# Kernel optimization log

Measured on AMD Instinct MI355X. Metric: run time of the kernel, lower is better.

## Reference

```python
import jax, jax.numpy as jnp
import numpy as np

N = 16384   # nodes
E = 131072  # edges (avg degree 8)
F = 64      # channels (hidden_irreps scalar multiplicity)
K = 16      # spherical harmonic components, l=0..3
Z = 10      # num_elements
G = 64      # graphs in batch
NB = 8      # num_bessel
RMAX = 5.0
P = 5       # num_polynomial_cutoff
AVG = 8.0   # avg_num_neighbors


def _sph(u):
    # real spherical harmonics l=0..3, 'component' normalization, unit input u [E,3]
    x, y, z = u[..., 0], u[..., 1], u[..., 2]
    s3, s5, s7 = 3.0 ** 0.5, 5.0 ** 0.5, 7.0 ** 0.5
    s15, s21, s35, s105 = 15.0 ** 0.5, 21.0 ** 0.5, 35.0 ** 0.5, 105.0 ** 0.5
    Y = [jnp.ones_like(x),
         s3 * x, s3 * y, s3 * z,
         s15 * x * y, s15 * y * z, 0.5 * s5 * (3.0 * z * z - 1.0), s15 * x * z,
         0.5 * s15 * (x * x - y * y),
         0.25 * s35 * y * (3.0 * x * x - y * y), 0.5 * s105 * x * y * z,
         0.25 * s21 * y * (5.0 * z * z - 1.0), 0.5 * s7 * z * (5.0 * z * z - 3.0),
         0.25 * s21 * x * (5.0 * z * z - 1.0), 0.25 * s105 * z * (x * x - y * y),
         0.25 * s35 * x * (x * x - 3.0 * y * y)]
    return jnp.stack(Y, axis=-1)  # [E,16]


def _radial(lengths):
    # Bessel basis * polynomial cutoff envelope (p=5)
    u = lengths / RMAX
    n = jnp.arange(1, NB + 1, dtype=lengths.dtype)
    safe = jnp.maximum(lengths, 1e-6)
    bess = (2.0 / RMAX) ** 0.5 * jnp.sin(n * jnp.pi * u[:, None]) / safe[:, None]
    env = (1.0 - 0.5 * (P + 1) * (P + 2) * u ** P + P * (P + 2) * u ** (P + 1)
           - 0.5 * P * (P + 1) * u ** (P + 2))
    env = env * (u < 1.0).astype(lengths.dtype)
    return bess * env[:, None]  # [E,NB]


def setup_inputs() -> dict:
    key = jax.random.key(0)
    ks = jax.random.split(key, 16)
    d = {}
    d['positions'] = jax.random.normal(ks[0], (N, 3), jnp.float32) * 1.5
    d['atomic_energies'] = jax.random.normal(ks[1], (Z,), jnp.float32)
    d['W_embed'] = jax.random.normal(ks[2], (Z, F), jnp.float32)
    d['rW1'] = jax.random.normal(ks[3], (2, NB, 64), jnp.float32) / NB ** 0.5
    d['rW2'] = jax.random.normal(ks[4], (2, 64, 64), jnp.float32) / 8.0
    d['rW3'] = jax.random.normal(ks[5], (2, 64, 64), jnp.float32) / 8.0
    d['rWout'] = jax.random.normal(ks[6], (2, 64, K * F), jnp.float32) / 8.0
    d['Wsc'] = jax.random.normal(ks[7], (2, Z, F, F), jnp.float32) / F ** 0.5
    d['pw'] = jax.random.normal(ks[8], (2, 3, F), jnp.float32) * 0.1
    d['read1_w'] = jax.random.normal(ks[9], (F,), jnp.float32) / F ** 0.5
    d['read2_Wa'] = jax.random.normal(ks[10], (F, 16), jnp.float32) / F ** 0.5
    d['read2_wb'] = jax.random.normal(ks[11], (16,), jnp.float32) / 4.0
    d['species'] = jax.random.randint(ks[12], (N,), 0, Z, jnp.int32)
    d['edge_index'] = jax.random.randint(ks[13], (2, E), 0, N, jnp.int32)
    d['batch'] = jnp.sort(jax.random.randint(ks[14], (N,), 0, G, jnp.int32))
    return d


def reference(positions, atomic_energies, W_embed, rW1, rW2, rW3, rWout, Wsc, pw,
              read1_w, read2_Wa, read2_wb, species, edge_index, batch):
    silu = jax.nn.silu
    src, dst = edge_index[0], edge_index[1]
    vec = positions[dst] - positions[src]                       # [E,3]
    lengths = jnp.sqrt(jnp.sum(vec * vec, axis=-1) + 1e-12)
    unit = vec / lengths[:, None]
    Y = _sph(unit)                                              # [E,K]
    edge_feats = _radial(lengths)                               # [E,NB]

    onehot = jax.nn.one_hot(species, Z, dtype=positions.dtype)  # node_attrs
    node_e0 = atomic_energies[species]                          # AtomicEnergiesBlock
    h = jnp.zeros((N, K, F), positions.dtype).at[:, 0, :].set(onehot @ W_embed)

    node_es = node_e0
    for l in range(2):  # num_interactions (structurally fixed small loop)
        # radial MLP [NB]->64->64->64->K*F, per-edge tensor-product weights
        R = silu(silu(silu(edge_feats @ rW1[l]) @ rW2[l]) @ rW3[l]) @ rWout[l]
        R = R.reshape(E, K, F)
        # gather -> channelwise tensor product with spherical harmonics -> scatter
        m = R * Y[:, :, None] * h[src, 0, :][:, None, :]        # [E,K,F]
        A = jax.ops.segment_sum(m, dst, num_segments=N) / AVG   # [N,K,F]
        # element-dependent skip connection (residual sc)
        sc = jnp.einsum('nkc,ncd->nkd', h, Wsc[l][species])
        # symmetric product basis (correlation up to 3) -> invariant contractions
        inv2 = jnp.sum(A * A, axis=1)                           # [N,F]
        inv3 = inv2 * A[:, 0, :]
        h_new = A * pw[l, 0][None, None, :]
        h_new = h_new.at[:, 0, :].add(inv2 * pw[l, 1] + inv3 * pw[l, 2])
        h = h_new + sc
        if l == 0:
            node_es = node_es + h[:, 0, :] @ read1_w            # LinearReadoutBlock
        else:
            node_es = node_es + silu(h[:, 0, :] @ read2_Wa) @ read2_wb  # NonLinearReadout
    total_energy = jax.ops.segment_sum(node_es, batch, num_segments=G)  # [G]
    return total_energy
```

## Files before the change

kernel.cpp:

```cpp
#include <hip/hip_runtime.h>
#include <math.h>


#define NN 16384
#define NE 131072
#define NZ 10
#define NG 64

typedef __attribute__((ext_vector_type(8))) short bf16x8;
typedef __attribute__((ext_vector_type(4))) float f32x4;

__device__ __forceinline__ float silu_f(float x) {
    return x / (1.0f + __expf(-x));
}

__device__ __forceinline__ unsigned short f2bf_rne(float x) {
    unsigned int u = __float_as_uint(x);
    unsigned int r = (u + 0x7FFFu + ((u >> 16) & 1u)) >> 16;
    return (unsigned short)r;
}
__device__ __forceinline__ float bf2f(unsigned short b) {
    return __uint_as_float(((unsigned int)b) << 16);
}

__global__ __launch_bounds__(256) void k_count(
    const int* __restrict__ ei, int* __restrict__ deg)
{
    int e = blockIdx.x * 256 + threadIdx.x;
    if (e < NE) atomicAdd(&deg[ei[NE + e]], 1);
}

__global__ __launch_bounds__(256) void k_scan(
    const int* __restrict__ deg, int* __restrict__ cursor)
{
    __shared__ int part[256];
    int t = threadIdx.x;
    int base = t * 64;
    int s = 0;
    for (int i = 0; i < 64; i++) s += deg[base + i];
    part[t] = s;
    __syncthreads();
    for (int off = 1; off < 256; off <<= 1) {
        int v = (t >= off) ? part[t - off] : 0;
        __syncthreads();
        part[t] += v;
        __syncthreads();
    }
    int run = (t > 0) ? part[t - 1] : 0;
    for (int i = 0; i < 64; i++) { cursor[base + i] = run; run += deg[base + i]; }
}

__global__ __launch_bounds__(256) void k_fill(
    const int* __restrict__ ei, int* __restrict__ cursor,
    int* __restrict__ sSrc, int* __restrict__ sDst)
{
    int e = blockIdx.x * 256 + threadIdx.x;
    if (e >= NE) return;
    int d = ei[NE + e];
    int p = atomicAdd(&cursor[d], 1);
    sSrc[p] = ei[e];
    sDst[p] = d;
}

__global__ __launch_bounds__(256) void k_wprep(
    const float* __restrict__ Wout, unsigned short* __restrict__ Bh,
    unsigned short* __restrict__ Bl)
{
    int idx = blockIdx.x * 256 + threadIdx.x;
    int lane = idx & 63;
    int nb = (idx >> 6) & 63;
    int ks = (idx >> 12) & 1;
    int layer = idx >> 13;
    int col = nb * 16 + (lane & 15);
    int tbase = ks * 32 + ((lane >> 4) << 3);
    #pragma unroll
    for (int j = 0; j < 8; j++) {
        float v = Wout[(size_t)layer * 65536 + (size_t)(tbase + j) * 1024 + col];
        unsigned short hi = f2bf_rne(v);
        unsigned short lo = f2bf_rne(v - bf2f(hi));
        Bh[(size_t)idx * 8 + j] = hi;
        Bl[(size_t)idx * 8 + j] = lo;
    }
}

__global__ __launch_bounds__(256) void k_edge_geom(
    const float* __restrict__ pos, const int* __restrict__ sSrc,
    const int* __restrict__ sDst, float* __restrict__ Y, float* __restrict__ feats)
{
    int e = blockIdx.x * 256 + threadIdx.x;
    if (e >= NE) return;
    int s = sSrc[e];
    int d = sDst[e];
    float vx = pos[d*3+0] - pos[s*3+0];
    float vy = pos[d*3+1] - pos[s*3+1];
    float vz = pos[d*3+2] - pos[s*3+2];
    float len = sqrtf(vx*vx + vy*vy + vz*vz + 1e-12f);
    float inv = 1.0f / len;
    float x = vx*inv, y = vy*inv, z = vz*inv;

    const float s3 = 1.7320508075688772f, s5 = 2.2360679774997896f;
    const float s7 = 2.6457513110645907f, s15 = 3.872983346207417f;
    const float s21 = 4.58257569495584f, s35 = 5.916079783099616f;
    const float s105 = 10.246950765959598f;
    float xx = x*x, yy = y*y, zz = z*z;
    float* Ye = Y + (size_t)e*16;
    Ye[0] = 1.0f;
    Ye[1] = s3*x; Ye[2] = s3*y; Ye[3] = s3*z;
    Ye[4] = s15*x*y; Ye[5] = s15*y*z; Ye[6] = 0.5f*s5*(3.0f*zz - 1.0f);
    Ye[7] = s15*x*z; Ye[8] = 0.5f*s15*(xx - yy);
    Ye[9]  = 0.25f*s35*y*(3.0f*xx - yy);
    Ye[10] = 0.5f*s105*x*y*z;
    Ye[11] = 0.25f*s21*y*(5.0f*zz - 1.0f);
    Ye[12] = 0.5f*s7*z*(5.0f*zz - 3.0f);
    Ye[13] = 0.25f*s21*x*(5.0f*zz - 1.0f);
    Ye[14] = 0.25f*s105*z*(xx - yy);
    Ye[15] = 0.25f*s35*x*(xx - 3.0f*yy);

    float u = len * 0.2f;
    float safe = fmaxf(len, 1e-6f);
    float u5 = u*u; u5 = u5*u5*u;
    float env = 1.0f - 21.0f*u5 + 35.0f*u5*u - 15.0f*u5*u*u;
    env = (u < 1.0f) ? env : 0.0f;
    float c = 0.6324555320336759f * env / safe;
    float* fe = feats + (size_t)e*8;
    const float PI = 3.14159265358979323846f;
    #pragma unroll
    for (int n = 1; n <= 8; n++)
        fe[n-1] = c * __sinf((float)n * PI * u);
}

__global__ __launch_bounds__(256) void k_h_init(
    const float* __restrict__ W_embed, const float* __restrict__ ae,
    const int* __restrict__ species, float* __restrict__ h0,
    float* __restrict__ node_es)
{
    int i = blockIdx.x * 256 + threadIdx.x;
    int n = i >> 6, r = i & 63;
    int sp = species[n];
    h0[i] = W_embed[sp*64 + r];
    if (r == 0) node_es[n] = ae[sp];
}

__global__ __launch_bounds__(256) void k_radial(
    const float* __restrict__ feats, const float* __restrict__ rW1,
    const float* __restrict__ rW2, const float* __restrict__ rW3,
    float* __restrict__ T3)
{
    __shared__ float w1[8*64];
    __shared__ float w2[64*64];
    __shared__ float w3[64*64];
    __shared__ float act[4][64];
    for (int i = threadIdx.x; i < 8*64; i += 256) w1[i] = rW1[i];
    for (int i = threadIdx.x; i < 64*64; i += 256) { w2[i] = rW2[i]; w3[i] = rW3[i]; }
    __syncthreads();
    int wave = threadIdx.x >> 6, lane = threadIdx.x & 63;
    for (int e0 = blockIdx.x * 4; e0 < NE; e0 += gridDim.x * 4) {
        int e = e0 + wave;
        const float* fe = feats + (size_t)e*8;
        float a = 0.f;
        #pragma unroll
        for (int i = 0; i < 8; i++) a = fmaf(fe[i], w1[i*64+lane], a);
        a = silu_f(a);
        act[wave][lane] = a;
        float b = 0.f;
        #pragma unroll
        for (int i = 0; i < 64; i++) b = fmaf(act[wave][i], w2[i*64+lane], b);
        b = silu_f(b);
        act[wave][lane] = b;
        float cc = 0.f;
        #pragma unroll
        for (int i = 0; i < 64; i++) cc = fmaf(act[wave][i], w3[i*64+lane], cc);
        T3[(size_t)e*64 + lane] = silu_f(cc);
    }
}

__global__ __launch_bounds__(256) void k_message(
    const float* __restrict__ T3, const unsigned short* __restrict__ Bh,
    const unsigned short* __restrict__ Bl, const float* __restrict__ Y,
    const float* __restrict__ h, const int* __restrict__ sSrc,
    const int* __restrict__ sDst, float* __restrict__ A)
{
    __shared__ float mbuf[16][518];
    __shared__ float hs[16][64];
    __shared__ float ys[16][16];
    __shared__ int srcs[16];
    __shared__ int dsts[16];

    int tid = threadIdx.x;
    int lane = tid & 63;
    int w = tid >> 6;
    int tile0 = blockIdx.x * 64;
    const bf16x8* Bhf = (const bf16x8*)Bh;
    const bf16x8* Blf = (const bf16x8*)Bl;

    int prev_d = -1, run_start = 0;
    float r00 = 0.f, r01 = 0.f, r10 = 0.f, r11 = 0.f;

    for (int sb = 0; sb < 4; sb++) {
        int g0 = tile0 + sb * 16;
        __syncthreads();
        if (tid < 16) { srcs[tid] = sSrc[g0 + tid]; dsts[tid] = sDst[g0 + tid]; }

        const float* trow = T3 + (size_t)(g0 + (lane & 15)) * 64 + ((lane >> 4) << 3);
        float4 p0 = *(const float4*)(trow);
        float4 p1 = *(const float4*)(trow + 4);
        float4 p2 = *(const float4*)(trow + 32);
        float4 p3 = *(const float4*)(trow + 36);
        bf16x8 ah0, al0, ah1, al1;
        {
            float v[16] = {p0.x,p0.y,p0.z,p0.w, p1.x,p1.y,p1.z,p1.w,
                           p2.x,p2.y,p2.z,p2.w, p3.x,p3.y,p3.z,p3.w};
            #pragma unroll
            for (int j = 0; j < 8; j++) {
                unsigned short hi = f2bf_rne(v[j]);
                ah0[j] = (short)hi;
                al0[j] = (short)f2bf_rne(v[j] - bf2f(hi));
            }
            #pragma unroll
            for (int j = 0; j < 8; j++) {
                unsigned short hi = f2bf_rne(v[8+j]);
                ah1[j] = (short)hi;
                al1[j] = (short)f2bf_rne(v[8+j] - bf2f(hi));
            }
        }
        __syncthreads();
        {
            int row = tid >> 4, q = tid & 15;
            ((float4*)hs[row])[q] = ((const float4*)(h + (size_t)srcs[row] * 64))[q];
            ys[row][q] = Y[(size_t)(g0 + row) * 16 + q];
        }
        __syncthreads();

        float hv[4][4];
        #pragma unroll
        for (int r = 0; r < 4; r++)
            #pragma unroll
            for (int m4 = 0; m4 < 4; m4++)
                hv[r][m4] = hs[(lane >> 4) * 4 + r][m4 * 16 + (lane & 15)];

        auto merge = [&](int p, float& r0, float& r1, int& pd_io, int& rs_io) {
            int pd = pd_io, rs = rs_io;
            #pragma unroll 1
            for (int e = 0; e < 16; e++) {
                int g = sb * 16 + e;
                int d = dsts[e];
                if (g == 0) {
                    pd = d;
                } else if (d != pd) {
                    float* Ap = A + (size_t)pd * 1024 + p * 512 + 2 * tid;
                    if (rs == 0) { atomicAdd(Ap, r0); atomicAdd(Ap + 1, r1); }
                    else         { *(float2*)Ap = make_float2(r0, r1); }
                    r0 = 0.f; r1 = 0.f; rs = g; pd = d;
                }
                float2 v = *(const float2*)&mbuf[e][2 * tid];
                r0 += v.x; r1 += v.y;
            }
            pd_io = pd; rs_io = rs;
        };

        for (int p = 0; p < 2; p++) {
            float yv[4][2];
            #pragma unroll
            for (int r = 0; r < 4; r++)
                #pragma unroll
                for (int kk = 0; kk < 2; kk++)
                    yv[r][kk] = ys[(lane >> 4) * 4 + r][p * 8 + w * 2 + kk] * 0.125f;

            #pragma unroll
            for (int nbl = 0; nbl < 8; nbl++) {
                int nb = p * 32 + w * 8 + nbl;
                bf16x8 bh0 = Bhf[(0 * 64 + nb) * 64 + lane];
                bf16x8 bl0 = Blf[(0 * 64 + nb) * 64 + lane];
                bf16x8 bh1 = Bhf[(1 * 64 + nb) * 64 + lane];
                bf16x8 bl1 = Blf[(1 * 64 + nb) * 64 + lane];
                f32x4 acc = {0.f, 0.f, 0.f, 0.f};
                acc = __builtin_amdgcn_mfma_f32_16x16x32_bf16(ah0, bh0, acc, 0, 0, 0);
                acc = __builtin_amdgcn_mfma_f32_16x16x32_bf16(al0, bh0, acc, 0, 0, 0);
                acc = __builtin_amdgcn_mfma_f32_16x16x32_bf16(ah0, bl0, acc, 0, 0, 0);
                acc = __builtin_amdgcn_mfma_f32_16x16x32_bf16(ah1, bh1, acc, 0, 0, 0);
                acc = __builtin_amdgcn_mfma_f32_16x16x32_bf16(al1, bh1, acc, 0, 0, 0);
                acc = __builtin_amdgcn_mfma_f32_16x16x32_bf16(ah1, bl1, acc, 0, 0, 0);
                #pragma unroll
                for (int r = 0; r < 4; r++) {
                    float m = acc[r] * yv[r][nbl >> 2] * hv[r][nbl & 3];
                    mbuf[(lane >> 4) * 4 + r][(w * 8 + nbl) * 16 + (lane & 15)] = m;
                }
            }
            __syncthreads();
            if (p == 0) {
                int pd0 = prev_d, rs0 = run_start;
                merge(0, r00, r01, pd0, rs0);
            } else {
                merge(1, r10, r11, prev_d, run_start);
            }
            __syncthreads();
        }
    }
    {
        float* Ap = A + (size_t)prev_d * 1024 + 2 * tid;
        atomicAdd(Ap, r00); atomicAdd(Ap + 1, r01);
        float* Ap1 = A + (size_t)prev_d * 1024 + 512 + 2 * tid;
        atomicAdd(Ap1, r10); atomicAdd(Ap1 + 1, r11);
    }
}

__global__ __launch_bounds__(256) void k_update0(
    const float* __restrict__ A, const float* __restrict__ h0,
    const float* __restrict__ Wsc, const float* __restrict__ pw,
    const float* __restrict__ read1_w, const int* __restrict__ species,
    float* __restrict__ h2, float* __restrict__ node_es)
{
    __shared__ float h0s[4][64];
    int wave = threadIdx.x >> 6, lane = threadIdx.x & 63;
    int n = blockIdx.x * 4 + wave;
    h0s[wave][lane] = h0[(size_t)n*64 + lane];
    __syncthreads();
    int sp = species[n];
    const float* W = Wsc + (size_t)sp*4096;
    float sc0 = 0.f;
    #pragma unroll
    for (int c = 0; c < 64; c++) sc0 = fmaf(h0s[wave][c], W[c*64+lane], sc0);
    float a[16], inv2 = 0.f;
    #pragma unroll
    for (int kk = 0; kk < 16; kk++) {
        a[kk] = A[(size_t)n*1024 + kk*64 + lane];
        inv2 = fmaf(a[kk], a[kk], inv2);
    }
    float inv3 = inv2 * a[0];
    float hn0 = a[0]*pw[lane] + inv2*pw[64+lane] + inv3*pw[128+lane] + sc0;
    h2[(size_t)n*64 + lane] = hn0;
    float r = hn0 * read1_w[lane];
    #pragma unroll
    for (int off = 32; off; off >>= 1) r += __shfl_down(r, off, 64);
    if (lane == 0) node_es[n] += r;
}

__global__ __launch_bounds__(256) void k_update1(
    const float* __restrict__ A, const float* __restrict__ h2,
    const float* __restrict__ Wsc, const float* __restrict__ pw,
    const float* __restrict__ Wa, const float* __restrict__ wb,
    const int* __restrict__ species, float* __restrict__ node_es)
{
    __shared__ float h0s[4][64];
    __shared__ float hns[4][64];
    int wave = threadIdx.x >> 6, lane = threadIdx.x & 63;
    int n = blockIdx.x * 4 + wave;
    h0s[wave][lane] = h2[(size_t)n*64 + lane];
    __syncthreads();
    int sp = species[n];
    const float* W = Wsc + (size_t)sp*4096;
    float sc0 = 0.f;
    #pragma unroll
    for (int c = 0; c < 64; c++) sc0 = fmaf(h0s[wave][c], W[c*64+lane], sc0);
    float a[16], inv2 = 0.f;
    #pragma unroll
    for (int kk = 0; kk < 16; kk++) {
        a[kk] = A[(size_t)n*1024 + kk*64 + lane];
        inv2 = fmaf(a[kk], a[kk], inv2);
    }
    float inv3 = inv2 * a[0];
    float hn0 = a[0]*pw[lane] + inv2*pw[64+lane] + inv3*pw[128+lane] + sc0;
    hns[wave][lane] = hn0;
    __syncthreads();
    float contrib = 0.f;
    if (lane < 16) {
        float aj = 0.f;
        #pragma unroll
        for (int f = 0; f < 64; f++) aj = fmaf(hns[wave][f], Wa[f*16+lane], aj);
        contrib = silu_f(aj) * wb[lane];
    }
    #pragma unroll
    for (int off = 8; off; off >>= 1) contrib += __shfl_down(contrib, off, 64);
    if (lane == 0) node_es[n] += contrib;
}

__global__ __launch_bounds__(256) void k_reduce(
    const float* __restrict__ node_es, const int* __restrict__ batch,
    float* __restrict__ out)
{
    __shared__ float bins[NG];
    if (threadIdx.x < NG) bins[threadIdx.x] = 0.f;
    __syncthreads();
    for (int n = blockIdx.x*256 + threadIdx.x; n < NN; n += gridDim.x*256)
        atomicAdd(&bins[batch[n]], node_es[n]);
    __syncthreads();
    if (threadIdx.x < NG) atomicAdd(&out[threadIdx.x], bins[threadIdx.x]);
}

extern "C" void kernel_launch(void* const* d_in, const int* in_sizes, int n_in,
                              void* d_out, int out_size, void* d_ws, size_t ws_size,
                              hipStream_t stream)
{
    const float* positions = (const float*)d_in[0];
    const float* atomic_energies = (const float*)d_in[1];
    const float* W_embed  = (const float*)d_in[2];
    const float* rW1      = (const float*)d_in[3];
    const float* rW2      = (const float*)d_in[4];
    const float* rW3      = (const float*)d_in[5];
    const float* rWout    = (const float*)d_in[6];
    const float* Wsc      = (const float*)d_in[7];
    const float* pw       = (const float*)d_in[8];
    const float* read1_w  = (const float*)d_in[9];
    const float* read2_Wa = (const float*)d_in[10];
    const float* read2_wb = (const float*)d_in[11];
    const int* species    = (const int*)d_in[12];
    const int* edge_index = (const int*)d_in[13];
    const int* batch      = (const int*)d_in[14];
    float* out = (float*)d_out;

    char* w = (char*)d_ws;
    float* Y     = (float*)w;  w += (size_t)NE*16*4;
    float* feats = (float*)w;  w += (size_t)NE*8*4;
    float* T3    = (float*)w;  w += (size_t)NE*64*4;
    float* h0    = (float*)w;  w += (size_t)NN*64*4;
    float* h2    = (float*)w;  w += (size_t)NN*64*4;
    float* A     = (float*)w;  w += (size_t)NN*1024*4;
    float* node_es = (float*)w; w += (size_t)NN*4;
    int* deg     = (int*)w;    w += (size_t)NN*4;
    int* cursor  = (int*)w;    w += (size_t)NN*4;
    int* sSrc    = (int*)w;    w += (size_t)NE*4;
    int* sDst    = (int*)w;    w += (size_t)NE*4;
    unsigned short* Bh = (unsigned short*)w; w += (size_t)2*8192*8*2;
    unsigned short* Bl = (unsigned short*)w; w += (size_t)2*8192*8*2;

    hipMemsetAsync(deg, 0, (size_t)NN*4, stream);
    k_count<<<NE/256, 256, 0, stream>>>(edge_index, deg);
    k_scan<<<1, 256, 0, stream>>>(deg, cursor);
    k_fill<<<NE/256, 256, 0, stream>>>(edge_index, cursor, sSrc, sDst);

    k_wprep<<<64, 256, 0, stream>>>(rWout, Bh, Bl);
    k_edge_geom<<<NE/256, 256, 0, stream>>>(positions, sSrc, sDst, Y, feats);
    k_h_init<<<NN*64/256, 256, 0, stream>>>(W_embed, atomic_energies, species, h0, node_es);

    hipMemsetAsync(A, 0, (size_t)NN*1024*4, stream);
    k_radial<<<2048, 256, 0, stream>>>(feats, rW1, rW2, rW3, T3);
    k_message<<<NE/64, 256, 0, stream>>>(T3, Bh, Bl, Y, h0, sSrc, sDst, A);
    k_update0<<<NN/4, 256, 0, stream>>>(A, h0, Wsc, pw, read1_w, species, h2, node_es);

    hipMemsetAsync(A, 0, (size_t)NN*1024*4, stream);
    k_radial<<<2048, 256, 0, stream>>>(feats, rW1 + 8*64, rW2 + 64*64, rW3 + 64*64, T3);
    k_message<<<NE/64, 256, 0, stream>>>(T3, Bh + (size_t)8192*8, Bl + (size_t)8192*8,
                                         Y, h2, sSrc, sDst, A);
    k_update1<<<NN/4, 256, 0, stream>>>(A, h2, Wsc + 10*4096, pw + 192,
                                        read2_Wa, read2_wb, species, node_es);

    hipMemsetAsync(d_out, 0, NG*sizeof(float), stream);
    k_reduce<<<64, 256, 0, stream>>>(node_es, batch, out);
}
```

Before: 726.6 us.

## Reduce message runs in registers via shuffles instead of LDS staging buffer

The 33KB LDS message buffer and its two-phase merge loop are removed. Destination runs over the 64-edge tile are now precomputed once, and each MFMA output is reduced into per-run register carries using cross-lane shuffles, then written or atomically added to A directly. Dropping the large LDS buffer allows a higher occupancy hint (launch_bounds 256,4) and removes several barriers per sub-block. In exchange it adds a serial run-scan loop with branching per MFMA tile, extra shuffles, and more narrow 16-lane global stores.

```diff
diff --git a/kernel.cpp b/kernel.cpp
--- a/kernel.cpp
+++ b/kernel.cpp
@@ -174,34 +174,55 @@
     }
 }
 
-__global__ __launch_bounds__(256) void k_message(
+__global__ __launch_bounds__(256, 4) void k_message(
     const float* __restrict__ T3, const unsigned short* __restrict__ Bh,
     const unsigned short* __restrict__ Bl, const float* __restrict__ Y,
     const float* __restrict__ h, const int* __restrict__ sSrc,
     const int* __restrict__ sDst, float* __restrict__ A)
 {
-    __shared__ float mbuf[16][518];
     __shared__ float hs[16][64];
     __shared__ float ys[16][16];
     __shared__ int srcs[16];
-    __shared__ int dsts[16];
+    __shared__ int dall[64];
+    __shared__ int runs_s[65];
+    __shared__ int runs_d[64];
+    __shared__ int nruns_sh;
 
     int tid = threadIdx.x;
     int lane = tid & 63;
     int w = tid >> 6;
+    int gq = lane >> 4;
+    int cl = lane & 15;
     int tile0 = blockIdx.x * 64;
     const bf16x8* Bhf = (const bf16x8*)Bh;
     const bf16x8* Blf = (const bf16x8*)Bl;
 
-    int prev_d = -1, run_start = 0;
-    float r00 = 0.f, r01 = 0.f, r10 = 0.f, r11 = 0.f;
+    if (tid < 64) dall[tid] = sDst[tile0 + tid];
+    __syncthreads();
+    if (tid == 0) {
+        int nr = 0, prev = -1;
+        for (int e = 0; e < 64; e++) {
+            int d = dall[e];
+            if (d != prev) { runs_s[nr] = e; runs_d[nr] = d; prev = d; nr++; }
+        }
+        runs_s[nr] = 64;
+        nruns_sh = nr;
+    }
+    __syncthreads();
+
+    float carry[2][8];
+    #pragma unroll
+    for (int p = 0; p < 2; p++)
+        #pragma unroll
+        for (int q = 0; q < 8; q++) carry[p][q] = 0.f;
+
+    int run_lo = 0;
 
     for (int sb = 0; sb < 4; sb++) {
-        int g0 = tile0 + sb * 16;
-        __syncthreads();
-        if (tid < 16) { srcs[tid] = sSrc[g0 + tid]; dsts[tid] = sDst[g0 + tid]; }
-
-        const float* trow = T3 + (size_t)(g0 + (lane & 15)) * 64 + ((lane >> 4) << 3);
+        int S = sb * 16;
+        int g0 = tile0 + S;
+
+        const float* trow = T3 + (size_t)(g0 + cl) * 64 + (gq << 3);
         float4 p0 = *(const float4*)(trow);
         float4 p1 = *(const float4*)(trow + 4);
         float4 p2 = *(const float4*)(trow + 32);
@@ -223,6 +244,9 @@
                 al1[j] = (short)f2bf_rne(v[8+j] - bf2f(hi));
             }
         }
+
+        __syncthreads();
+        if (tid < 16) srcs[tid] = sSrc[g0 + tid];
         __syncthreads();
         {
             int row = tid >> 4, q = tid & 15;
@@ -236,43 +260,26 @@
         for (int r = 0; r < 4; r++)
             #pragma unroll
             for (int m4 = 0; m4 < 4; m4++)
-                hv[r][m4] = hs[(lane >> 4) * 4 + r][m4 * 16 + (lane & 15)];
-
-        auto merge = [&](int p, float& r0, float& r1, int& pd_io, int& rs_io) {
-            int pd = pd_io, rs = rs_io;
-            #pragma unroll 1
-            for (int e = 0; e < 16; e++) {
-                int g = sb * 16 + e;
-                int d = dsts[e];
-                if (g == 0) {
-                    pd = d;
-                } else if (d != pd) {
-                    float* Ap = A + (size_t)pd * 1024 + p * 512 + 2 * tid;
-                    if (rs == 0) { atomicAdd(Ap, r0); atomicAdd(Ap + 1, r1); }
-                    else         { *(float2*)Ap = make_float2(r0, r1); }
-                    r0 = 0.f; r1 = 0.f; rs = g; pd = d;
-                }
-                float2 v = *(const float2*)&mbuf[e][2 * tid];
-                r0 += v.x; r1 += v.y;
-            }
-            pd_io = pd; rs_io = rs;
-        };
-
+                hv[r][m4] = hs[gq*4 + r][m4*16 + cl];
+
+        while (runs_s[run_lo + 1] <= S) run_lo++;
+
+        #pragma unroll
         for (int p = 0; p < 2; p++) {
             float yv[4][2];
             #pragma unroll
             for (int r = 0; r < 4; r++)
                 #pragma unroll
                 for (int kk = 0; kk < 2; kk++)
-                    yv[r][kk] = ys[(lane >> 4) * 4 + r][p * 8 + w * 2 + kk] * 0.125f;
+                    yv[r][kk] = ys[gq*4 + r][p*8 + w*2 + kk] * 0.125f;
 
             #pragma unroll
             for (int nbl = 0; nbl < 8; nbl++) {
-                int nb = p * 32 + w * 8 + nbl;
-                bf16x8 bh0 = Bhf[(0 * 64 + nb) * 64 + lane];
-                bf16x8 bl0 = Blf[(0 * 64 + nb) * 64 + lane];
-                bf16x8 bh1 = Bhf[(1 * 64 + nb) * 64 + lane];
-                bf16x8 bl1 = Blf[(1 * 64 + nb) * 64 + lane];
+                int nb = p*32 + w*8 + nbl;
+                bf16x8 bh0 = Bhf[(0*64 + nb)*64 + lane];
+                bf16x8 bl0 = Blf[(0*64 + nb)*64 + lane];
+                bf16x8 bh1 = Bhf[(1*64 + nb)*64 + lane];
+                bf16x8 bl1 = Blf[(1*64 + nb)*64 + lane];
                 f32x4 acc = {0.f, 0.f, 0.f, 0.f};
                 acc = __builtin_amdgcn_mfma_f32_16x16x32_bf16(ah0, bh0, acc, 0, 0, 0);
                 acc = __builtin_amdgcn_mfma_f32_16x16x32_bf16(al0, bh0, acc, 0, 0, 0);
@@ -280,27 +287,43 @@
                 acc = __builtin_amdgcn_mfma_f32_16x16x32_bf16(ah1, bh1, acc, 0, 0, 0);
                 acc = __builtin_amdgcn_mfma_f32_16x16x32_bf16(al1, bh1, acc, 0, 0, 0);
                 acc = __builtin_amdgcn_mfma_f32_16x16x32_bf16(ah1, bl1, acc, 0, 0, 0);
-                #pragma unroll
-                for (int r = 0; r < 4; r++) {
-                    float m = acc[r] * yv[r][nbl >> 2] * hv[r][nbl & 3];
-                    mbuf[(lane >> 4) * 4 + r][(w * 8 + nbl) * 16 + (lane & 15)] = m;
+
+                float m0 = acc[0] * yv[0][nbl >> 2] * hv[0][nbl & 3];
+                float m1 = acc[1] * yv[1][nbl >> 2] * hv[1][nbl & 3];
+                float m2 = acc[2] * yv[2][nbl >> 2] * hv[2][nbl & 3];
+                float m3 = acc[3] * yv[3][nbl >> 2] * hv[3][nbl & 3];
+                int base = gq * 4;
+
+                int ri = run_lo;
+                #pragma unroll 1
+                while (runs_s[ri] < S + 16) {
+                    int s = runs_s[ri] - S;
+                    int e = runs_s[ri + 1] - S;
+                    float part = 0.f;
+                    part += (base+0 >= s && base+0 < e) ? m0 : 0.f;
+                    part += (base+1 >= s && base+1 < e) ? m1 : 0.f;
+                    part += (base+2 >= s && base+2 < e) ? m2 : 0.f;
+                    part += (base+3 >= s && base+3 < e) ? m3 : 0.f;
+                    carry[p][nbl] += part;
+                    if (e <= 16) {
+                        float t = carry[p][nbl];
+                        t += __shfl_xor(t, 16, 64);
+                        t += __shfl_xor(t, 32, 64);
+                        carry[p][nbl] = 0.f;
+                        if (lane < 16) {
+                            int gs = runs_s[ri];
+                            int ge = runs_s[ri + 1];
+                            float* Ap = A + (size_t)runs_d[ri] * 1024 + nb * 16 + cl;
+                            if (gs == 0 || ge == 64) atomicAdd(Ap, t);
+                            else *Ap = t;
+                        }
+                        ri++;
+                    } else {
+                        break;
+                    }
                 }
             }
-            __syncthreads();
-            if (p == 0) {
-                int pd0 = prev_d, rs0 = run_start;
-                merge(0, r00, r01, pd0, rs0);
-            } else {
-                merge(1, r10, r11, prev_d, run_start);
-            }
-            __syncthreads();
         }
-    }
-    {
-        float* Ap = A + (size_t)prev_d * 1024 + 2 * tid;
-        atomicAdd(Ap, r00); atomicAdd(Ap + 1, r01);
-        float* Ap1 = A + (size_t)prev_d * 1024 + 512 + 2 * tid;
-        atomicAdd(Ap1, r10); atomicAdd(Ap1 + 1, r11);
     }
 }
 
```

Measured after the change: 1.675 ms. 131% more time.
